# Kernel optimization log

Hardware: AMD Instinct MI355X
Metric: run time of the kernel (lower is better)

The kernel has to match this reference:

```python
import jax, jax.numpy as jnp
import numpy as np

EPS = 1e-05
SINKHORN_ITERS = 20


def sinkhorn_knopp(M):
    M = jnp.exp(M)
    def body(_, M):
        M = M / (M.sum(axis=1, keepdims=True) + EPS)
        M = M / (M.sum(axis=0, keepdims=True) + EPS)
        return M
    return jax.lax.fori_loop(0, SINKHORN_ITERS, body, M)


def setup_inputs() -> dict:
    key = jax.random.key(0)
    k1, k2 = jax.random.split(key)
    B, n, C = 4096, 4, 4096
    alpha_init = 0.01
    return {
        "x_expanded": jax.random.normal(k1, (B, n, C), dtype=jnp.float32),
        "rmsnorm_weight": jnp.ones((C,), dtype=jnp.float32),
        "H_pre": jnp.zeros((n,), dtype=jnp.float32),
        "H_post": jnp.zeros((n,), dtype=jnp.float32),
        "H_res": alpha_init * jax.random.normal(k2, (n, n), dtype=jnp.float32),
    }


def reference(x_expanded, rmsnorm_weight, H_pre, H_post, H_res):
    B, n, C = x_expanded.shape
    H_pre_act = jax.nn.sigmoid(H_pre)            # (n,)
    H_post_act = 2.0 * jax.nn.sigmoid(H_post)    # (n,)
    M = sinkhorn_knopp(H_res)                    # (n, n) doubly-stochastic-ish

    # aggregate across expansion dim: (B, C)
    x_agg = jnp.einsum('i,bic->bc', H_pre_act, x_expanded)
    # RMSNorm over C
    rms = jnp.sqrt(jnp.mean(x_agg * x_agg, axis=-1, keepdims=True) + EPS)
    x_normed = x_agg / rms * rmsnorm_weight      # (B, C)

    y_dist = H_post_act[None, :, None] * x_normed[:, None, :]  # (B, n, C)
    x_mixed = jnp.einsum('ij,bjc->bic', M, x_expanded)          # (B, n, C)
    return x_mixed + y_dist
```

## Files before the change

kernel.cpp:

```cpp
#include <hip/hip_runtime.h>
#include <math.h>

#define EPSF 1e-5f
#define SINKHORN_ITERS 20
#define C_DIM 4096
#define N_DIM 4

typedef __attribute__((ext_vector_type(4))) float fx4;

__global__ void prep_kernel(const float* __restrict__ H_pre,
                            const float* __restrict__ H_post,
                            const float* __restrict__ H_res,
                            float* __restrict__ params) {
    if (threadIdx.x != 0 || blockIdx.x != 0) return;
    float M[4][4];
    for (int i = 0; i < 4; ++i)
        for (int j = 0; j < 4; ++j)
            M[i][j] = expf(H_res[i * 4 + j]);
    for (int it = 0; it < SINKHORN_ITERS; ++it) {
        for (int i = 0; i < 4; ++i) {
            float s = M[i][0] + M[i][1] + M[i][2] + M[i][3] + EPSF;
            M[i][0] /= s; M[i][1] /= s; M[i][2] /= s; M[i][3] /= s;
        }
        for (int j = 0; j < 4; ++j) {
            float s = M[0][j] + M[1][j] + M[2][j] + M[3][j] + EPSF;
            M[0][j] /= s; M[1][j] /= s; M[2][j] /= s; M[3][j] /= s;
        }
    }
    for (int i = 0; i < 4; ++i) {
        params[i]     = 1.0f / (1.0f + expf(-H_pre[i]));
        params[4 + i] = 2.0f / (1.0f + expf(-H_post[i]));
    }
    for (int i = 0; i < 4; ++i)
        for (int j = 0; j < 4; ++j)
            params[8 + i * 4 + j] = M[i][j];
}

__global__ __launch_bounds__(512, 8)
void fused_kernel(const float* __restrict__ x,
                  const float* __restrict__ w,
                  const float* __restrict__ params,
                  float* __restrict__ out) {
    const int b = blockIdx.x;
    const int t = threadIdx.x;

    const float p0 = params[0], p1 = params[1], p2 = params[2], p3 = params[3];

    const size_t base = (size_t)b * (N_DIM * C_DIM);
    const int c0 = t * 4;

    fx4 xv[4][2];
    #pragma unroll
    for (int i = 0; i < 4; ++i)
        #pragma unroll
        for (int k = 0; k < 2; ++k)
            xv[i][k] = __builtin_nontemporal_load(
                reinterpret_cast<const fx4*>(x + base + i * C_DIM + k * 2048 + c0));

    float ss = 0.0f;
    #pragma unroll
    for (int k = 0; k < 2; ++k) {
        fx4 a = p0 * xv[0][k] + p1 * xv[1][k] + p2 * xv[2][k] + p3 * xv[3][k];
        ss += a.x * a.x + a.y * a.y + a.z * a.z + a.w * a.w;
    }

    #pragma unroll
    for (int off = 32; off > 0; off >>= 1)
        ss += __shfl_down(ss, off, 64);
    __shared__ float sp[8];
    if ((t & 63) == 0) sp[t >> 6] = ss;
    __syncthreads();
    const float tot = sp[0] + sp[1] + sp[2] + sp[3]
                    + sp[4] + sp[5] + sp[6] + sp[7];
    const float inv = 1.0f / sqrtf(tot * (1.0f / (float)C_DIM) + EPSF);

    #pragma unroll
    for (int k = 0; k < 2; ++k) {
        fx4 wv = *reinterpret_cast<const fx4*>(w + k * 2048 + c0);
        fx4 a = p0 * xv[0][k] + p1 * xv[1][k] + p2 * xv[2][k] + p3 * xv[3][k];
        fx4 nw = a * inv * wv;
        #pragma unroll
        for (int i = 0; i < 4; ++i) {
            const float m0 = params[8 + i * 4 + 0];
            const float m1 = params[8 + i * 4 + 1];
            const float m2 = params[8 + i * 4 + 2];
            const float m3 = params[8 + i * 4 + 3];
            const float po = params[4 + i];
            fx4 o = m0 * xv[0][k] + m1 * xv[1][k] + m2 * xv[2][k] + m3 * xv[3][k]
                  + po * nw;
            __builtin_nontemporal_store(
                o, reinterpret_cast<fx4*>(out + base + i * C_DIM + k * 2048 + c0));
        }
    }
}

extern "C" void kernel_launch(void* const* d_in, const int* in_sizes, int n_in,
                              void* d_out, int out_size, void* d_ws, size_t ws_size,
                              hipStream_t stream) {
    const float* x      = (const float*)d_in[0];
    const float* w      = (const float*)d_in[1];
    const float* H_pre  = (const float*)d_in[2];
    const float* H_post = (const float*)d_in[3];
    const float* H_res  = (const float*)d_in[4];
    float* out    = (float*)d_out;
    float* params = (float*)d_ws;

    const int B = in_sizes[0] / (N_DIM * C_DIM);

    prep_kernel<<<1, 64, 0, stream>>>(H_pre, H_post, H_res, params);
    fused_kernel<<<B, 512, 0, stream>>>(x, w, params, out);
}
```

Measured before the change: 114.6 us.

## Fuse Sinkhorn parameter prep into main kernel and drop nontemporal memory ops

Removes the single-thread prep kernel and has every thread recompute the Sinkhorn-normalized mixing matrix and sigmoid gates in registers, after issuing its input loads. This eliminates a separate launch and the dependency on a workspace parameter buffer. It also replaces nontemporal loads/stores with plain ones and lowers the launch-bounds occupancy hint, trading redundant per-thread ALU work and register pressure for fewer launches.

```diff
diff --git a/kernel.cpp b/kernel.cpp
--- a/kernel.cpp
+++ b/kernel.cpp
@@ -8,43 +8,15 @@
 
 typedef __attribute__((ext_vector_type(4))) float fx4;
 
-__global__ void prep_kernel(const float* __restrict__ H_pre,
-                            const float* __restrict__ H_post,
-                            const float* __restrict__ H_res,
-                            float* __restrict__ params) {
-    if (threadIdx.x != 0 || blockIdx.x != 0) return;
-    float M[4][4];
-    for (int i = 0; i < 4; ++i)
-        for (int j = 0; j < 4; ++j)
-            M[i][j] = expf(H_res[i * 4 + j]);
-    for (int it = 0; it < SINKHORN_ITERS; ++it) {
-        for (int i = 0; i < 4; ++i) {
-            float s = M[i][0] + M[i][1] + M[i][2] + M[i][3] + EPSF;
-            M[i][0] /= s; M[i][1] /= s; M[i][2] /= s; M[i][3] /= s;
-        }
-        for (int j = 0; j < 4; ++j) {
-            float s = M[0][j] + M[1][j] + M[2][j] + M[3][j] + EPSF;
-            M[0][j] /= s; M[1][j] /= s; M[2][j] /= s; M[3][j] /= s;
-        }
-    }
-    for (int i = 0; i < 4; ++i) {
-        params[i]     = 1.0f / (1.0f + expf(-H_pre[i]));
-        params[4 + i] = 2.0f / (1.0f + expf(-H_post[i]));
-    }
-    for (int i = 0; i < 4; ++i)
-        for (int j = 0; j < 4; ++j)
-            params[8 + i * 4 + j] = M[i][j];
-}
-
-__global__ __launch_bounds__(512, 8)
+__global__ __launch_bounds__(512, 4)
 void fused_kernel(const float* __restrict__ x,
                   const float* __restrict__ w,
-                  const float* __restrict__ params,
+                  const float* __restrict__ H_pre,
+                  const float* __restrict__ H_post,
+                  const float* __restrict__ H_res,
                   float* __restrict__ out) {
     const int b = blockIdx.x;
     const int t = threadIdx.x;
-
-    const float p0 = params[0], p1 = params[1], p2 = params[2], p3 = params[3];
 
     const size_t base = (size_t)b * (N_DIM * C_DIM);
     const int c0 = t * 4;
@@ -54,8 +26,35 @@
     for (int i = 0; i < 4; ++i)
         #pragma unroll
         for (int k = 0; k < 2; ++k)
-            xv[i][k] = __builtin_nontemporal_load(
-                reinterpret_cast<const fx4*>(x + base + i * C_DIM + k * 2048 + c0));
+            xv[i][k] = *reinterpret_cast<const fx4*>(
+                x + base + i * C_DIM + k * 2048 + c0);
+
+    float M[4][4];
+    #pragma unroll
+    for (int i = 0; i < 4; ++i)
+        #pragma unroll
+        for (int j = 0; j < 4; ++j)
+            M[i][j] = __expf(H_res[i * 4 + j]);
+    for (int it = 0; it < SINKHORN_ITERS; ++it) {
+        #pragma unroll
+        for (int i = 0; i < 4; ++i) {
+            float s = 1.0f / (M[i][0] + M[i][1] + M[i][2] + M[i][3] + EPSF);
+            M[i][0] *= s; M[i][1] *= s; M[i][2] *= s; M[i][3] *= s;
+        }
+        #pragma unroll
+        for (int j = 0; j < 4; ++j) {
+            float s = 1.0f / (M[0][j] + M[1][j] + M[2][j] + M[3][j] + EPSF);
+            M[0][j] *= s; M[1][j] *= s; M[2][j] *= s; M[3][j] *= s;
+        }
+    }
+    const float p0 = 1.0f / (1.0f + __expf(-H_pre[0]));
+    const float p1 = 1.0f / (1.0f + __expf(-H_pre[1]));
+    const float p2 = 1.0f / (1.0f + __expf(-H_pre[2]));
+    const float p3 = 1.0f / (1.0f + __expf(-H_pre[3]));
+    float po[4];
+    #pragma unroll
+    for (int i = 0; i < 4; ++i)
+        po[i] = 2.0f / (1.0f + __expf(-H_post[i]));
 
     float ss = 0.0f;
     #pragma unroll
@@ -81,15 +80,10 @@
         fx4 nw = a * inv * wv;
         #pragma unroll
         for (int i = 0; i < 4; ++i) {
-            const float m0 = params[8 + i * 4 + 0];
-            const float m1 = params[8 + i * 4 + 1];
-            const float m2 = params[8 + i * 4 + 2];
-            const float m3 = params[8 + i * 4 + 3];
-            const float po = params[4 + i];
-            fx4 o = m0 * xv[0][k] + m1 * xv[1][k] + m2 * xv[2][k] + m3 * xv[3][k]
-                  + po * nw;
-            __builtin_nontemporal_store(
-                o, reinterpret_cast<fx4*>(out + base + i * C_DIM + k * 2048 + c0));
+            fx4 o = M[i][0] * xv[0][k] + M[i][1] * xv[1][k]
+                  + M[i][2] * xv[2][k] + M[i][3] * xv[3][k]
+                  + po[i] * nw;
+            *reinterpret_cast<fx4*>(out + base + i * C_DIM + k * 2048 + c0) = o;
         }
     }
 }
@@ -102,11 +96,9 @@
     const float* H_pre  = (const float*)d_in[2];
     const float* H_post = (const float*)d_in[3];
     const float* H_res  = (const float*)d_in[4];
-    float* out    = (float*)d_out;
-    float* params = (float*)d_ws;
+    float* out = (float*)d_out;
 
     const int B = in_sizes[0] / (N_DIM * C_DIM);
 
-    prep_kernel<<<1, 64, 0, stream>>>(H_pre, H_post, H_res, params);
-    fused_kernel<<<B, 512, 0, stream>>>(x, w, params, out);
+    fused_kernel<<<B, 512, 0, stream>>>(x, w, H_pre, H_post, H_res, out);
 }
```

Result: slower. 165.3 us (+44.2%).
